# Kernel tuning notes

Hardware: AMD Instinct MI355X
Metric: run time of the kernel (lower is better)

Reference implementation:

```python
import jax, jax.numpy as jnp
import numpy as np

NLAYERS = 4
HEADS = 4
HEAD_DIM = 64
C = HEADS * HEAD_DIM  # 256
MAX_LEN = 1024


def setup_inputs() -> dict:
    key = jax.random.key(0)
    k1, k2, k3 = jax.random.split(key, 3)
    B, S = 16, 1024
    x = jax.random.normal(k1, (B, C, 1, S), dtype=jnp.float32)
    # length is only used via its static shape[0]; values are irrelevant
    length = jnp.zeros((MAX_LEN,), dtype=jnp.int32)
    # per-layer 1x1 conv weights, std=0.1 as in the torch init (squeeze the 1x1 spatial dims)
    w = jax.random.normal(k2, (NLAYERS, C, C), dtype=jnp.float32) * 0.1
    # persistent kv buffer
    kv = jax.random.normal(k3, (NLAYERS, HEADS, MAX_LEN, HEAD_DIM), dtype=jnp.float32) * 0.1
    return {"x": x, "length": length, "w": w, "kv": kv}


def reference(x, length, w, kv):
    B, _, _, S = x.shape
    L = length.shape[0]  # static slice length into kv buffer
    scale = 1.0 / jnp.sqrt(jnp.asarray(HEAD_DIM, dtype=x.dtype))
    for i in range(NLAYERS):
        # 1x1 conv == channel projection: (B,C,1,S) -> (B,C,1,S)
        x = jnp.einsum('oc,bchs->bohs', w[i], x)
        # view (B,4,64,S) then permute -> query (B,H,S,D)
        q = x.reshape(B, HEADS, HEAD_DIM, S).transpose(0, 1, 3, 2)
        kvi = kv[i, :, :L]  # (H, L, D); broadcasts over batch like the (1,H,L,D) torch slice
        # scaled dot-product attention with k == v == kvi
        scores = jnp.einsum('bhsd,hld->bhsl', q, kvi) * scale
        attn = jax.nn.softmax(scores, axis=-1)
        o = jnp.einsum('bhsl,hld->bhsd', attn, kvi)  # (B,H,S,D)
        # permute back and merge heads -> (B,256,1,S)
        x = o.transpose(0, 1, 3, 2).reshape(B, C, 1, S)
    return x
```

## Files before the change

### kernel.cpp

```cpp
#include <hip/hip_runtime.h>

#define NL   4
#define NH   4
#define HD   64
#define CD   256
#define SQL  1024
#define BB   16

typedef _Float16 half8 __attribute__((ext_vector_type(8)));
typedef _Float16 half4 __attribute__((ext_vector_type(4)));
typedef _Float16 half2v __attribute__((ext_vector_type(2)));
typedef float    f32x4 __attribute__((ext_vector_type(4)));
typedef float    f32x16 __attribute__((ext_vector_type(16)));
typedef unsigned short u16x8 __attribute__((ext_vector_type(8)));
typedef unsigned int  uint4v __attribute__((ext_vector_type(4)));

static __device__ __forceinline__ float bf2f(unsigned short u) {
    union { unsigned int i; float f; } v; v.i = ((unsigned int)u) << 16; return v.f;
}
static __device__ __forceinline__ unsigned short f2bf(float f) {
    union { float f; unsigned int i; } v; v.f = f;
    unsigned int u = v.i;
    return (unsigned short)((u + 0x7fffu + ((u >> 16) & 1u)) >> 16);
}

static __device__ __forceinline__ int detect_flag(const void* win) {
    const uint4v* w = (const uint4v*)win;
    int cnt = 0;
    uint4v u[16];
#pragma unroll
    for (int i = 0; i < 16; i++) u[i] = w[i];
#pragma unroll
    for (int i = 0; i < 16; i++)
#pragma unroll
        for (int j = 0; j < 4; j++) {
            unsigned int lo = u[i][j] & 0xFFFFu;
            int e = (int)((lo >> 7) & 0xFF);
            cnt += (e >= 96 && e <= 144) ? 1 : 0;
        }
    return cnt >= 48 ? 1 : 0;
}

__global__ __launch_bounds__(256) void prep_all(const void* __restrict__ xin,
                                                const void* __restrict__ win,
                                                const void* __restrict__ kvin,
                                                _Float16* __restrict__ x16,
                                                _Float16* __restrict__ w16,
                                                _Float16* __restrict__ kaF,
                                                _Float16* __restrict__ vtF,
                                                int* __restrict__ flagp) {
    __shared__ __align__(16) _Float16 tile[64][72];
    const int bi = blockIdx.x;
    const int t = threadIdx.x;
    const int isbf = detect_flag(win);

    if (bi < 1024) {
        const int st = bi & 15, ct = (bi >> 4) & 3, b = bi >> 6;
        const int r = t >> 2, seg = t & 3;
        const size_t base = ((size_t)(b * CD + ct * 64 + r)) * SQL + st * 64 + seg * 16;
        float v[16];
        if (isbf) {
            const unsigned short* src = (const unsigned short*)xin + base;
            u16x8 u0 = *(const u16x8*)(src);
            u16x8 u1 = *(const u16x8*)(src + 8);
#pragma unroll
            for (int j = 0; j < 8; j++) { v[j] = bf2f(u0[j]); v[8 + j] = bf2f(u1[j]); }
        } else {
            const float* src = (const float*)xin + base;
#pragma unroll
            for (int c = 0; c < 4; c++) {
                f32x4 a = *(const f32x4*)(src + c * 4);
#pragma unroll
                for (int j = 0; j < 4; j++) v[c * 4 + j] = a[j];
            }
        }
#pragma unroll
        for (int j = 0; j < 16; j++) tile[r][seg * 16 + j] = (_Float16)v[j];
        __syncthreads();
        half8 o0, o1;
#pragma unroll
        for (int j = 0; j < 8; j++) { o0[j] = tile[seg * 16 + j][r]; o1[j] = tile[seg * 16 + 8 + j][r]; }
        _Float16* dt = x16 + ((size_t)(b * SQL + st * 64 + r)) * CD + ct * 64 + seg * 16;
        *(half8*)(dt) = o0;
        *(half8*)(dt + 8) = o1;
    } else if (bi < 1280) {
        const int j2 = bi - 1024;
        const int lt = j2 & 15, ih = j2 >> 4;
        const int r = t >> 2, seg = t & 3;
        const size_t base = ((size_t)(ih * SQL + lt * 64 + r)) * HD + seg * 16;
        float v[16];
        if (isbf) {
            const unsigned short* src = (const unsigned short*)kvin + base;
            u16x8 u0 = *(const u16x8*)(src);
            u16x8 u1 = *(const u16x8*)(src + 8);
#pragma unroll
            for (int j = 0; j < 8; j++) { v[j] = bf2f(u0[j]); v[8 + j] = bf2f(u1[j]); }
        } else {
            const float* src = (const float*)kvin + base;
#pragma unroll
            for (int c = 0; c < 4; c++) {
                f32x4 a = *(const f32x4*)(src + c * 4);
#pragma unroll
                for (int j = 0; j < 4; j++) v[c * 4 + j] = a[j];
            }
        }
#pragma unroll
        for (int j = 0; j < 16; j++) tile[r][seg * 16 + j] = (_Float16)v[j];
        __syncthreads();
        const int l = t & 63, hie = l >> 5, lne = l & 31;
        _Float16* kaB = kaF + ((size_t)ih << 16);
        _Float16* vtB = vtF + ((size_t)ih << 16);
#pragma unroll
        for (int it = 0; it < 2; it++) {
            const int c = (t >> 6) + it * 4;
            half8 ok = *(const half8*)(&tile[(c >> 2) * 32 + lne][(c & 3) * 16 + hie * 8]);
            half8 ov;
#pragma unroll
            for (int j = 0; j < 8; j++)
                ov[j] = tile[(c & 3) * 16 + hie * 8 + j][(c >> 2) * 32 + lne];
            *(half8*)(kaB + ((lt * 8 + c) << 9) + l * 8) = ok;
            *(half8*)(vtB + ((lt * 8 + c) << 9) + l * 8) = ov;
        }
    } else {
        if (bi == 1280 && t == 0) *flagp = isbf;
        const int i = (bi - 1280) * 256 + t;
        const size_t base = (size_t)i * 8;
        half8 h;
        if (isbf) {
            u16x8 u = *(const u16x8*)((const unsigned short*)win + base);
#pragma unroll
            for (int j = 0; j < 8; j++) h[j] = (_Float16)bf2f(u[j]);
        } else {
            const float* p = (const float*)win + base;
            f32x4 a0 = *(const f32x4*)(p);
            f32x4 a1 = *(const f32x4*)(p + 4);
#pragma unroll
            for (int j = 0; j < 4; j++) { h[j] = (_Float16)a0[j]; h[4 + j] = (_Float16)a1[j]; }
        }
        *(half8*)(w16 + base) = h;
    }
}

__global__ __launch_bounds__(256) void layer_fused(const _Float16* __restrict__ xg,
                                                   _Float16* __restrict__ xout,
                                                   const _Float16* __restrict__ w16,
                                                   const _Float16* __restrict__ kaF,
                                                   const _Float16* __restrict__ vtF,
                                                   const int* __restrict__ flagp,
                                                   void* __restrict__ outp,
                                                   int L) {
    const int sb = blockIdx.x;
    const int h  = blockIdx.y;
    const int b  = blockIdx.z;
    const int t  = threadIdx.x;
    const int wv = t >> 6, lane = t & 63, ln = lane & 31, hi = lane >> 5;
    const int s0 = sb * 128 + wv * 32;

    const int isbf_final = (L == NL - 1) ? *flagp : 0;

    const _Float16* kaB = kaF + ((size_t)(L * NH + h) << 16) + lane * 8;
    const _Float16* vtB = vtF + ((size_t)(L * NH + h) << 16) + lane * 8;

    f32x16 gacc[2];
#pragma unroll
    for (int dblk = 0; dblk < 2; dblk++)
#pragma unroll
        for (int r = 0; r < 16; r++) gacc[dblk][r] = 0.0f;
    const _Float16* wb = w16 + ((size_t)L << 16) + ((size_t)(h * 64) << 8);
#pragma unroll
    for (int kc = 0; kc < 16; kc++) {
        half8 bx = *(const half8*)(xg + ((size_t)((b << 10) + s0 + ln) << 8) + kc * 16 + hi * 8);
#pragma unroll
        for (int dblk = 0; dblk < 2; dblk++) {
            half8 aw = *(const half8*)(wb + ((size_t)(dblk * 32 + ln) << 8) + kc * 16 + hi * 8);
            gacc[dblk] = __builtin_amdgcn_mfma_f32_32x32x16_f16(aw, bx, gacc[dblk], 0, 0, 0);
        }
    }

    const float sc = 0.180336880111120f;
    half8 qb[4];
#pragma unroll
    for (int dblk = 0; dblk < 2; dblk++)
#pragma unroll
        for (int k1 = 0; k1 < 2; k1++) {
            unsigned int u01 = __builtin_bit_cast(unsigned int,
                __builtin_amdgcn_cvt_pkrtz(gacc[dblk][k1 * 8 + 0] * sc, gacc[dblk][k1 * 8 + 1] * sc));
            unsigned int u23 = __builtin_bit_cast(unsigned int,
                __builtin_amdgcn_cvt_pkrtz(gacc[dblk][k1 * 8 + 2] * sc, gacc[dblk][k1 * 8 + 3] * sc));
            unsigned int w01 = __builtin_bit_cast(unsigned int,
                __builtin_amdgcn_cvt_pkrtz(gacc[dblk][k1 * 8 + 4] * sc, gacc[dblk][k1 * 8 + 5] * sc));
            unsigned int w23 = __builtin_bit_cast(unsigned int,
                __builtin_amdgcn_cvt_pkrtz(gacc[dblk][k1 * 8 + 6] * sc, gacc[dblk][k1 * 8 + 7] * sc));
            asm("v_permlane32_swap_b32 %0, %1" : "+v"(u01), "+v"(w01));
            asm("v_permlane32_swap_b32 %0, %1" : "+v"(u23), "+v"(w23));
            uint4v q; q[0] = u01; q[1] = u23; q[2] = w01; q[3] = w23;
            qb[dblk * 2 + k1] = __builtin_bit_cast(half8, q);
        }

    f32x16 oacc[2];
#pragma unroll
    for (int dblk = 0; dblk < 2; dblk++)
#pragma unroll
        for (int r = 0; r < 16; r++) oacc[dblk][r] = 0.0f;
    f32x4 rsum;
#pragma unroll
    for (int r = 0; r < 4; r++) rsum[r] = 0.0f;

    auto process = [&](const half8* ka, const half8* va) {
        f32x16 stt[2];
#pragma unroll
        for (int lblk = 0; lblk < 2; lblk++)
#pragma unroll
            for (int r = 0; r < 16; r++) stt[lblk][r] = 0.0f;
        __builtin_amdgcn_s_setprio(1);
#pragma unroll
        for (int lblk = 0; lblk < 2; lblk++)
#pragma unroll
            for (int kd = 0; kd < 4; kd++)
                stt[lblk] = __builtin_amdgcn_mfma_f32_32x32x16_f16(
                    ka[lblk * 4 + kd], qb[kd], stt[lblk], 0, 0, 0);
        __builtin_amdgcn_s_setprio(0);

        half8 pb[4];
#pragma unroll
        for (int lblk = 0; lblk < 2; lblk++) {
            float e[16];
#pragma unroll
            for (int r = 0; r < 16; r++) e[r] = __builtin_amdgcn_exp2f(stt[lblk][r]);
#pragma unroll
            for (int g = 0; g < 4; g++)
                rsum[g] += (e[g * 4 + 0] + e[g * 4 + 1]) + (e[g * 4 + 2] + e[g * 4 + 3]);
#pragma unroll
            for (int k1 = 0; k1 < 2; k1++) {
                unsigned int u01 = __builtin_bit_cast(unsigned int,
                    __builtin_amdgcn_cvt_pkrtz(e[k1 * 8 + 0], e[k1 * 8 + 1]));
                unsigned int u23 = __builtin_bit_cast(unsigned int,
                    __builtin_amdgcn_cvt_pkrtz(e[k1 * 8 + 2], e[k1 * 8 + 3]));
                unsigned int w01 = __builtin_bit_cast(unsigned int,
                    __builtin_amdgcn_cvt_pkrtz(e[k1 * 8 + 4], e[k1 * 8 + 5]));
                unsigned int w23 = __builtin_bit_cast(unsigned int,
                    __builtin_amdgcn_cvt_pkrtz(e[k1 * 8 + 6], e[k1 * 8 + 7]));
                asm("v_permlane32_swap_b32 %0, %1" : "+v"(u01), "+v"(w01));
                asm("v_permlane32_swap_b32 %0, %1" : "+v"(u23), "+v"(w23));
                uint4v p; p[0] = u01; p[1] = u23; p[2] = w01; p[3] = w23;
                pb[lblk * 2 + k1] = __builtin_bit_cast(half8, p);
            }
        }

        __builtin_amdgcn_s_setprio(1);
#pragma unroll
        for (int dblk = 0; dblk < 2; dblk++)
#pragma unroll
            for (int ks = 0; ks < 4; ks++)
                oacc[dblk] = __builtin_amdgcn_mfma_f32_32x32x16_f16(
                    va[dblk * 4 + ks], pb[ks], oacc[dblk], 0, 0, 0);
        __builtin_amdgcn_s_setprio(0);
    };

#define LOADK(dst, lt)                                                        \
    do {                                                                      \
        _Pragma("unroll")                                                     \
        for (int c = 0; c < 8; c++)                                           \
            dst[c] = *(const half8*)(kaB + (((lt) * 8 + c) << 9));            \
    } while (0)
#define LOADV(dst, lt)                                                        \
    do {                                                                      \
        _Pragma("unroll")                                                     \
        for (int c = 0; c < 8; c++)                                           \
            dst[c] = *(const half8*)(vtB + (((lt) * 8 + c) << 9));            \
    } while (0)

    half8 ka0[8], ka1[8], va[8];
    LOADK(ka0, 0);
    LOADV(va, 0);

#pragma unroll 1
    for (int lt = 0; lt < 16; lt += 2) {
        LOADK(ka1, lt + 1);
        process(ka0, va);
        LOADV(va, lt + 1);
        if (lt + 2 < 16) LOADK(ka0, lt + 2);
        process(ka1, va);
        if (lt + 2 < 16) LOADV(va, lt + 2);
    }
#undef LOADK
#undef LOADV

    float rs = (rsum[0] + rsum[1]) + (rsum[2] + rsum[3]);
    unsigned int ra = __builtin_bit_cast(unsigned int, rs);
    unsigned int rb = ra;
    asm("" : "+v"(rb));
    asm("v_permlane32_swap_b32 %0, %1" : "+v"(ra), "+v"(rb));
    const float inv = 1.0f / (__builtin_bit_cast(float, ra) + __builtin_bit_cast(float, rb));
    const int s = s0 + ln;

    if (L < NL - 1) {
#pragma unroll
        for (int dblk = 0; dblk < 2; dblk++)
#pragma unroll
            for (int q2 = 0; q2 < 4; q2++) {
                half4 hv;
#pragma unroll
                for (int r = 0; r < 4; r++) hv[r] = (_Float16)(oacc[dblk][q2 * 4 + r] * inv);
                *(half4*)(xout + (((size_t)((b << 10) + s)) << 8) +
                          (h << 6) + dblk * 32 + q2 * 8 + hi * 4) = hv;
            }
    } else if (isbf_final) {
#pragma unroll
        for (int dblk = 0; dblk < 2; dblk++)
#pragma unroll
            for (int q2 = 0; q2 < 4; q2++)
#pragma unroll
                for (int r = 0; r < 4; r++) {
                    const int c = (h << 6) + dblk * 32 + q2 * 8 + hi * 4 + r;
                    ((unsigned short*)outp)[(((size_t)(b * CD + c)) << 10) + s] =
                        f2bf(oacc[dblk][q2 * 4 + r] * inv);
                }
    } else {
#pragma unroll
        for (int dblk = 0; dblk < 2; dblk++)
#pragma unroll
            for (int q2 = 0; q2 < 4; q2++)
#pragma unroll
                for (int r = 0; r < 4; r++) {
                    const int c = (h << 6) + dblk * 32 + q2 * 8 + hi * 4 + r;
                    ((float*)outp)[(((size_t)(b * CD + c)) << 10) + s] =
                        oacc[dblk][q2 * 4 + r] * inv;
                }
    }
}

extern "C" void kernel_launch(void* const* d_in, const int* in_sizes, int n_in,
                              void* d_out, int out_size, void* d_ws, size_t ws_size,
                              hipStream_t stream) {
    const void* xin = d_in[0];
    const void* win = d_in[2];
    const void* kvin = d_in[3];

    char* ws = (char*)d_ws;
    const size_t MB = 1u << 20;
    _Float16* xa  = (_Float16*)(ws);
    _Float16* xb  = (_Float16*)(ws + 8 * MB);
    _Float16* w16 = (_Float16*)(ws + 16 * MB);
    _Float16* kaF = (_Float16*)(ws + 17 * MB);
    _Float16* vtF = (_Float16*)(ws + 19 * MB);
    int*      flg = (int*)(ws + 21 * MB);

    prep_all<<<dim3(1024 + 256 + 128), 256, 0, stream>>>(xin, win, kvin, xa, w16, kaF, vtF, flg);

    _Float16* cur = xa;
    _Float16* nxt = xb;
    for (int i = 0; i < NL; i++) {
        layer_fused<<<dim3(SQL / 128, NH, BB), 256, 0, stream>>>(cur, nxt, w16, kaF, vtF,
                                                                 flg, d_out, i);
        _Float16* tmp = cur; cur = nxt; nxt = tmp;
    }
}
```

Before: 216.1 us.

## Split KV length across two wave groups and merge partial attention via LDS

Doubles the block to 512 threads so that two wave groups each process half of the key/value tiles for the same query rows. The second group writes its unnormalized output accumulator and row sum to shared memory, and the first group adds them in before normalizing and storing. This halves the serial KV loop per wave and adds more waves in flight to hide latency. The cost is a barrier, LDS traffic, and a duplicated projection step per wave group. The merge without a max rescale relies on softmax having no running-max correction.

```diff
diff --git a/kernel.cpp b/kernel.cpp
--- a/kernel.cpp
+++ b/kernel.cpp
@@ -141,20 +141,23 @@
     }
 }
 
-__global__ __launch_bounds__(256) void layer_fused(const _Float16* __restrict__ xg,
-                                                   _Float16* __restrict__ xout,
-                                                   const _Float16* __restrict__ w16,
-                                                   const _Float16* __restrict__ kaF,
-                                                   const _Float16* __restrict__ vtF,
-                                                   const int* __restrict__ flagp,
-                                                   void* __restrict__ outp,
-                                                   int L) {
+__global__ __launch_bounds__(512, 2) void layer_fused(const _Float16* __restrict__ xg,
+                                                      _Float16* __restrict__ xout,
+                                                      const _Float16* __restrict__ w16,
+                                                      const _Float16* __restrict__ kaF,
+                                                      const _Float16* __restrict__ vtF,
+                                                      const int* __restrict__ flagp,
+                                                      void* __restrict__ outp,
+                                                      int L) {
+    __shared__ __align__(16) float scr[9472];
     const int sb = blockIdx.x;
     const int h  = blockIdx.y;
     const int b  = blockIdx.z;
     const int t  = threadIdx.x;
     const int wv = t >> 6, lane = t & 63, ln = lane & 31, hi = lane >> 5;
-    const int s0 = sb * 128 + wv * 32;
+    const int sg = wv & 3, hl = wv >> 2;
+    const int s0 = sb * 128 + sg * 32;
+    const int lt0 = hl * 8;
 
     const int isbf_final = (L == NL - 1) ? *flagp : 0;
 
@@ -271,62 +274,81 @@
     } while (0)
 
     half8 ka0[8], ka1[8], va[8];
-    LOADK(ka0, 0);
-    LOADV(va, 0);
+    LOADK(ka0, lt0);
+    LOADV(va, lt0);
 
 #pragma unroll 1
-    for (int lt = 0; lt < 16; lt += 2) {
-        LOADK(ka1, lt + 1);
+    for (int i = 0; i < 8; i += 2) {
+        LOADK(ka1, lt0 + i + 1);
         process(ka0, va);
-        LOADV(va, lt + 1);
-        if (lt + 2 < 16) LOADK(ka0, lt + 2);
+        LOADV(va, lt0 + i + 1);
+        if (i + 2 < 8) LOADK(ka0, lt0 + i + 2);
         process(ka1, va);
-        if (lt + 2 < 16) LOADV(va, lt + 2);
+        if (i + 2 < 8) LOADV(va, lt0 + i + 2);
     }
 #undef LOADK
 #undef LOADV
 
     float rs = (rsum[0] + rsum[1]) + (rsum[2] + rsum[3]);
-    unsigned int ra = __builtin_bit_cast(unsigned int, rs);
-    unsigned int rb = ra;
-    asm("" : "+v"(rb));
-    asm("v_permlane32_swap_b32 %0, %1" : "+v"(ra), "+v"(rb));
-    const float inv = 1.0f / (__builtin_bit_cast(float, ra) + __builtin_bit_cast(float, rb));
-    const int s = s0 + ln;
-
-    if (L < NL - 1) {
+    const int sidx = (sg * 64 + lane) * 37;
+
+    if (hl == 1) {
 #pragma unroll
         for (int dblk = 0; dblk < 2; dblk++)
 #pragma unroll
-            for (int q2 = 0; q2 < 4; q2++) {
-                half4 hv;
-#pragma unroll
-                for (int r = 0; r < 4; r++) hv[r] = (_Float16)(oacc[dblk][q2 * 4 + r] * inv);
-                *(half4*)(xout + (((size_t)((b << 10) + s)) << 8) +
-                          (h << 6) + dblk * 32 + q2 * 8 + hi * 4) = hv;
-            }
-    } else if (isbf_final) {
+            for (int r = 0; r < 16; r++) scr[sidx + dblk * 16 + r] = oacc[dblk][r];
+        scr[sidx + 32] = rs;
+    }
+    __syncthreads();
+
+    if (hl == 0) {
 #pragma unroll
         for (int dblk = 0; dblk < 2; dblk++)
 #pragma unroll
-            for (int q2 = 0; q2 < 4; q2++)
-#pragma unroll
-                for (int r = 0; r < 4; r++) {
-                    const int c = (h << 6) + dblk * 32 + q2 * 8 + hi * 4 + r;
-                    ((unsigned short*)outp)[(((size_t)(b * CD + c)) << 10) + s] =
-                        f2bf(oacc[dblk][q2 * 4 + r] * inv);
+            for (int r = 0; r < 16; r++) oacc[dblk][r] += scr[sidx + dblk * 16 + r];
+        rs += scr[sidx + 32];
+
+        unsigned int ra = __builtin_bit_cast(unsigned int, rs);
+        unsigned int rb = ra;
+        asm("" : "+v"(rb));
+        asm("v_permlane32_swap_b32 %0, %1" : "+v"(ra), "+v"(rb));
+        const float inv = 1.0f / (__builtin_bit_cast(float, ra) + __builtin_bit_cast(float, rb));
+        const int s = s0 + ln;
+
+        if (L < NL - 1) {
+#pragma unroll
+            for (int dblk = 0; dblk < 2; dblk++)
+#pragma unroll
+                for (int q2 = 0; q2 < 4; q2++) {
+                    half4 hv;
+#pragma unroll
+                    for (int r = 0; r < 4; r++) hv[r] = (_Float16)(oacc[dblk][q2 * 4 + r] * inv);
+                    *(half4*)(xout + (((size_t)((b << 10) + s)) << 8) +
+                              (h << 6) + dblk * 32 + q2 * 8 + hi * 4) = hv;
                 }
-    } else {
-#pragma unroll
-        for (int dblk = 0; dblk < 2; dblk++)
-#pragma unroll
-            for (int q2 = 0; q2 < 4; q2++)
-#pragma unroll
-                for (int r = 0; r < 4; r++) {
-                    const int c = (h << 6) + dblk * 32 + q2 * 8 + hi * 4 + r;
-                    ((float*)outp)[(((size_t)(b * CD + c)) << 10) + s] =
-                        oacc[dblk][q2 * 4 + r] * inv;
-                }
+        } else if (isbf_final) {
+#pragma unroll
+            for (int dblk = 0; dblk < 2; dblk++)
+#pragma unroll
+                for (int q2 = 0; q2 < 4; q2++)
+#pragma unroll
+                    for (int r = 0; r < 4; r++) {
+                        const int c = (h << 6) + dblk * 32 + q2 * 8 + hi * 4 + r;
+                        ((unsigned short*)outp)[(((size_t)(b * CD + c)) << 10) + s] =
+                            f2bf(oacc[dblk][q2 * 4 + r] * inv);
+                    }
+        } else {
+#pragma unroll
+            for (int dblk = 0; dblk < 2; dblk++)
+#pragma unroll
+                for (int q2 = 0; q2 < 4; q2++)
+#pragma unroll
+                    for (int r = 0; r < 4; r++) {
+                        const int c = (h << 6) + dblk * 32 + q2 * 8 + hi * 4 + r;
+                        ((float*)outp)[(((size_t)(b * CD + c)) << 10) + s] =
+                            oacc[dblk][q2 * 4 + r] * inv;
+                    }
+        }
     }
 }
 
@@ -351,7 +373,7 @@
     _Float16* cur = xa;
     _Float16* nxt = xb;
     for (int i = 0; i < NL; i++) {
-        layer_fused<<<dim3(SQL / 128, NH, BB), 256, 0, stream>>>(cur, nxt, w16, kaF, vtF,
+        layer_fused<<<dim3(SQL / 128, NH, BB), 512, 0, stream>>>(cur, nxt, w16, kaF, vtF,
                                                                  flg, d_out, i);
         _Float16* tmp = cur; cur = nxt; nxt = tmp;
     }
```

After: 254.4 us. 17.7% more time.
